# Optimization experiments

Measured on AMD Instinct MI355X. Metric: run time of the kernel, lower is better.

Reference implementation:

```python
import jax, jax.numpy as jnp
import numpy as np


def setup_inputs() -> dict:
    key = jax.random.key(0)
    ks = jax.random.split(key, 8)
    B, De, Do, T, H, W = 4, 128, 512, 4, 30, 52
    s = 0.05  # weight init scale
    return {
        "m_in": jax.random.normal(ks[0], (B, De, T, H, W), jnp.float32),
        "m_out": jax.random.normal(ks[1], (B, Do, T, H, W), jnp.float32),
        "q_in": jax.random.normal(ks[2], (B, De, H, W), jnp.float32),
        "q_out": jax.random.normal(ks[3], (B, Do, H, W), jnp.float32),
        "wr": jax.random.normal(ks[4], (Do, 2 * Do), jnp.float32) * s,
        "br": jnp.zeros((Do,), jnp.float32),
        "wu": jax.random.normal(ks[5], (Do, 2 * Do), jnp.float32) * s,
        "bu": jnp.zeros((Do,), jnp.float32),
        "wc": jax.random.normal(ks[6], (Do, 2 * Do), jnp.float32) * s,
        "bc": jnp.zeros((Do,), jnp.float32),
    }


def reference(m_in, m_out, q_in, q_out, wr, br, wu, bu, wc, bc):
    B, De, T, H, W = m_in.shape
    Do = m_out.shape[1]
    PROP_LAYERS = 5

    # --- memory read: pairwise frame attention (bmm + softmax + bmm) ---
    # keys: all T memory frames flattened; queries: current frame.
    mi = m_in.reshape(B, De, T * H * W)            # [B, De, THW]
    qi = q_in.reshape(B, De, H * W)                # [B, De, HW]
    p = jnp.einsum('bdk,bdq->bkq', mi, qi) / (De ** 0.5)  # [B, THW, HW]
    p = jax.nn.softmax(p, axis=1)                  # softmax over memory locations (dim=1 in torch)
    mem = jnp.einsum('bok,bkq->boq', m_out.reshape(B, Do, T * H * W), p)
    mem = mem.reshape(B, Do, H, W)                 # mem_mean; identical every propagate layer

    # --- ConvGRU_h (kernel_size=1 => per-pixel linear gates) ---
    def conv1x1(w, b, x):
        return jnp.einsum('oc,bchw->bohw', w, x) + b[None, :, None, None]

    def gru(x, h):
        xh = jnp.concatenate([x, h], axis=1)                       # [B, 2*Do, H, W]
        r = jax.nn.sigmoid(conv1x1(wr, br, xh))
        u = jax.nn.sigmoid(conv1x1(wu, bu, xh))
        c = jnp.tanh(conv1x1(wc, bc, jnp.concatenate([x, r * h], axis=1)))
        return h * (1.0 - u) + u * c

    q0 = q_out
    q = q_out
    for _ in range(PROP_LAYERS):
        q = gru(q, mem)  # original: q_out = ConvGRU_h(q_out, mem_mean)
    return jnp.concatenate([q, q0], axis=1)  # [B, 2*Do, H, W]
```

## Files before the change

### kernel.cpp

```cpp
#include <hip/hip_runtime.h>
#include <hip/hip_bf16.h>
#include <math.h>

typedef unsigned short u16;
typedef __attribute__((ext_vector_type(8))) short bf16x8;
typedef __attribute__((ext_vector_type(4))) float f32x4;

__device__ __forceinline__ u16 f2bf(float f) {
  union { float f; unsigned u; } x; x.f = f;
  unsigned r = x.u + 0x7fffu + ((x.u >> 16) & 1u);
  return (u16)(r >> 16);
}
__device__ __forceinline__ float bf2f(u16 h) {
  union { unsigned u; float f; } x; x.u = ((unsigned)h) << 16;
  return x.f;
}
__device__ __forceinline__ float sigmf(float x) {
  x = fminf(fmaxf(x, -30.f), 30.f);
  return 1.f / (1.f + __expf(-x));
}
__device__ __forceinline__ float tanh_fast(float x) {
  x = fminf(fmaxf(x, -15.f), 15.f);
  float t = __expf(2.f * x);
  return (t - 1.f) / (t + 1.f);
}

template<int N> __device__ __forceinline__ void wait_vmcnt() {
  if constexpr (N == 0)       asm volatile("s_waitcnt vmcnt(0)" ::: "memory");
  else if constexpr (N == 4)  asm volatile("s_waitcnt vmcnt(4)" ::: "memory");
  else if constexpr (N == 6)  asm volatile("s_waitcnt vmcnt(6)" ::: "memory");
  else if constexpr (N == 8)  asm volatile("s_waitcnt vmcnt(8)" ::: "memory");
  else static_assert(N == 0, "add vmcnt case");
}

#define NB 4
#define DE 128
#define DO_ 512
#define HW 1560
#define THW 6240
#define NP 1664
#define KP 6272
#define PROP 5
#define PVSPLIT 4
#define PVKC 1568
#define SCALE 0.08838834764831845f

template<int MODE, int BMT, int BKT>
__device__ __forceinline__
void gemm_core(const u16* __restrict__ A, const u16* __restrict__ Bt,
               int K, int lda, int ldb, long a_bs, long b_bs,
               void* __restrict__ out0v, long o0_bs, int ld0,
               u16* __restrict__ out1, long o1_bs, int ld1,
               u16* __restrict__ out2, long o2_bs,
               const void* __restrict__ e0v, long e0_bs,
               const void* __restrict__ e1v, long e1_bs,
               const void* __restrict__ e2v, long e2_bs,
               const void* __restrict__ e3v, long e3_bs,
               int nvalid, float scale)
{
  constexpr int WR = BMT / 64;
  constexpr int WC = 4 / WR;
  constexpr int NF = 8 / WC;
  constexpr int KK = BKT / 32;
  constexpr int ASLOT = BMT * BKT / 8;
  constexpr int BSLOT = 128 * BKT / 8;
  constexpr int NISS = (ASLOT + BSLOT) / 256;
  constexpr int RSH = (BMT == 128) ? 7 : 6;
  __shared__ u16 lds[2][ASLOT + BSLOT][8];

  const int tid = threadIdx.x;
  const int wave = tid >> 6, lane = tid & 63;
  const int kg = lane >> 4, lr = lane & 15;
  const int wrw = wave / WC, wcw = wave % WC;
  const long b = blockIdx.z;
  const int m0 = blockIdx.x * BMT, n0 = blockIdx.y * 128;
  A += b * a_bs; Bt += b * b_bs;

  float* out0f = (float*)out0v;
  u16* out0h = (u16*)out0v;
  const float* e0f = (const float*)e0v;
  const u16* e0h = (const u16*)e0v;
  const u16* e1h = (const u16*)e1v;
  const u16* e2h = (const u16*)e2v;
  const u16* e3h = (const u16*)e3v;

  auto stage = [&](int buf, int kt) {
#pragma unroll
    for (int i = 0; i < NISS; ++i) {
      int s = tid + 256 * i;
      const u16* src;
      if (s < ASLOT) {
        int row = s & (BMT - 1), g = s >> RSH;
        src = A + (long)(m0 + row) * lda + kt + g * 8;
      } else {
        int s2 = s - ASLOT;
        int row = s2 & 127, g = s2 >> 7;
        src = Bt + (long)(n0 + row) * ldb + kt + g * 8;
      }
      __builtin_amdgcn_global_load_lds(
          (const __attribute__((address_space(1))) void*)src,
          (__attribute__((address_space(3))) void*)&lds[buf][wave * 64 + 256 * i][0],
          16, 0, 0);
    }
  };

  f32x4 acc[4][NF];
#pragma unroll
  for (int m = 0; m < 4; ++m)
#pragma unroll
    for (int n = 0; n < NF; ++n) acc[m][n] = (f32x4){0.f, 0.f, 0.f, 0.f};

  const int nt = K / BKT;
  stage(0, 0);
  for (int t = 0; t < nt; ++t) {
    int cur = t & 1;
    if (t + 1 < nt) {
      stage(cur ^ 1, (t + 1) * BKT);
      wait_vmcnt<NISS>();
    } else {
      wait_vmcnt<0>();
    }
    __builtin_amdgcn_s_barrier();
    bf16x8 af[KK][4], bfr[KK][NF];
#pragma unroll
    for (int kk = 0; kk < KK; ++kk) {
#pragma unroll
      for (int m = 0; m < 4; ++m)
        af[kk][m] = *(const bf16x8*)&lds[cur][(kk * 4 + kg) * BMT + wrw * 64 + m * 16 + lr][0];
#pragma unroll
      for (int n = 0; n < NF; ++n)
        bfr[kk][n] = *(const bf16x8*)&lds[cur][ASLOT + (kk * 4 + kg) * 128 + (wcw * NF + n) * 16 + lr][0];
    }
#pragma unroll
    for (int kk = 0; kk < KK; ++kk)
#pragma unroll
      for (int m = 0; m < 4; ++m)
#pragma unroll
        for (int n = 0; n < NF; ++n)
          acc[m][n] = __builtin_amdgcn_mfma_f32_16x16x32_bf16(af[kk][m], bfr[kk][n], acc[m][n], 0, 0, 0);
    __builtin_amdgcn_s_barrier();
  }

#pragma unroll
  for (int m = 0; m < 4; ++m) {
    int rloc = wrw * 64 + m * 16 + kg * 4;
#pragma unroll
    for (int n = 0; n < NF; ++n) {
      int col = n0 + (wcw * NF + n) * 16 + lr;
#pragma unroll
      for (int j = 0; j < 4; ++j) {
        long row = m0 + rloc + j;
        float v = acc[m][n][j];
        if constexpr (MODE == 2) {
          out1[b * o1_bs + row * ld1 + col] = f2bf(v + e0f[col]);
        } else if constexpr (MODE == 3) {
          if (col < 1024) {
            float gt = sigmf(v + bf2f(e0h[b * e0_bs + row * 1024 + col]));
            if (col < 512)
              out1[b * o1_bs + row * ld1 + 512 + col] =
                  f2bf(gt * bf2f(e1h[b * e1_bs + row * 512 + col]));
            else
              out0h[b * o0_bs + row * ld0 + (col - 512)] = f2bf(gt);
          } else {
            out2[b * o2_bs + row * 512 + (col - 1024)] = f2bf(v);
          }
        } else if constexpr (MODE == 4) {
          float cg = tanh_fast(v + bf2f(e3h[b * e3_bs + row * 512 + col]) + e0f[col]);
          float u = bf2f(e1h[b * e1_bs + row * 512 + col]);
          float mm = bf2f(e2h[b * e2_bs + row * 512 + col]);
          float x = mm * (1.f - u) + u * cg;
          out1[b * o1_bs + row * ld1 + col] = f2bf(x);
          if (out0f && row < nvalid)
            out0f[b * o0_bs + (long)col * ld0 + row] = x;
        }
      }
    }
  }
}

#define GEMM_ARGS                                                              \
  const u16* __restrict__ A, const u16* __restrict__ Bt, int K, int lda,       \
  int ldb, long a_bs, long b_bs, void* __restrict__ out0v, long o0_bs,         \
  int ld0, u16* __restrict__ out1, long o1_bs, int ld1,                        \
  u16* __restrict__ out2, long o2_bs,                                          \
  const void* __restrict__ e0v, long e0_bs, const void* __restrict__ e1v,      \
  long e1_bs, const void* __restrict__ e2v, long e2_bs,                        \
  const void* __restrict__ e3v, long e3_bs, int nvalid, float scale
#define GEMM_PASS A, Bt, K, lda, ldb, a_bs, b_bs, out0v, o0_bs, ld0, out1,     \
  o1_bs, ld1, out2, o2_bs, e0v, e0_bs, e1v, e1_bs, e2v, e2_bs, e3v, e3_bs,     \
  nvalid, scale

__global__ __launch_bounds__(256) void gk_chru(GEMM_ARGS)   { gemm_core<2, 64, 64>(GEMM_PASS); }
__global__ __launch_bounds__(256) void gk_gates(GEMM_ARGS)  { gemm_core<3, 128, 64>(GEMM_PASS); }
__global__ __launch_bounds__(256) void gk_cand(GEMM_ARGS)   { gemm_core<4, 64, 64>(GEMM_PASS); }

__global__ __launch_bounds__(256, 2)
void gemm_fa(const u16* __restrict__ qiT, const u16* __restrict__ miT,
             const u16* __restrict__ moutb,
             u16* __restrict__ Ppart, float* __restrict__ Zp)
{
  const int bid = blockIdx.x;
  const int xcd = bid & 7, i = bid >> 3;
  const int s = xcd * 52 + i;
  const int pair = s / 26, mb = s - pair * 26;
  const int b = pair >> 2, z = pair & 3;
  const int m0 = mb * 64;
  const int k0 = z * PVKC;

  const int tid = threadIdx.x;
  const int wave = tid >> 6, lane = tid & 63;
  const int kg = lane >> 4, lr = lane & 15;

  __shared__ u16 ldsQ[1024 * 8];
  __shared__ u16 ldsK[2][512 * 8];
  __shared__ u16 ldsP[64 * 40];

  const u16* Qb = qiT + (long)b * NP * DE;
  const u16* Mb = miT + (long)b * KP * DE;
  const u16* B0 = moutb + (long)b * DO_ * KP +
                  (long)(wave * 128 + lr) * KP + kg * 8;

  auto stageK = [&](int buf, int ts) {
#pragma unroll
    for (int i2 = 0; i2 < 2; ++i2) {
      int s2 = tid + 256 * i2;
      int row = s2 & 31, g = s2 >> 5;
      const u16* src = Mb + (long)(k0 + ts * 32 + row) * DE + g * 8;
      __builtin_amdgcn_global_load_lds(
          (const __attribute__((address_space(1))) void*)src,
          (__attribute__((address_space(3))) void*)&ldsK[buf][(wave * 64 + 256 * i2) * 8],
          16, 0, 0);
    }
  };

#pragma unroll
  for (int i2 = 0; i2 < 4; ++i2) {
    int s2 = tid + 256 * i2;
    int row = s2 & 63, g = s2 >> 6;
    const u16* src = Qb + (long)(m0 + row) * DE + g * 8;
    __builtin_amdgcn_global_load_lds(
        (const __attribute__((address_space(1))) void*)src,
        (__attribute__((address_space(3))) void*)&ldsQ[(wave * 64 + 256 * i2) * 8],
        16, 0, 0);
  }
  stageK(0, 0);
  __syncthreads();

  f32x4 acc[4][8];
#pragma unroll
  for (int m = 0; m < 4; ++m)
#pragma unroll
    for (int n = 0; n < 8; ++n) acc[m][n] = (f32x4){0.f, 0.f, 0.f, 0.f};
  float zacc[4] = {0.f, 0.f, 0.f, 0.f};
  bf16x8 b_[8];

#define FA_STEP(T, CUR, DOS)                                                     \
  {                                                                              \
    _Pragma("unroll") for (int n = 0; n < 8; ++n)                                \
        b_[n] = *(const bf16x8*)&B0[(long)n * 16 * KP + k0 + (T) * 32];          \
    if (DOS) stageK((CUR) ^ 1, (T) + 1);                                         \
    bf16x8 qf[4], kc[2][4];                                                      \
    _Pragma("unroll") for (int kk = 0; kk < 4; ++kk)                             \
        qf[kk] = *(const bf16x8*)&ldsQ[((kk * 4 + kg) * 64 + wave * 16 + lr) * 8]; \
    _Pragma("unroll") for (int n = 0; n < 2; ++n)                                \
        _Pragma("unroll") for (int kk = 0; kk < 4; ++kk)                         \
            kc[n][kk] = *(const bf16x8*)&ldsK[CUR][((kk * 4 + kg) * 32 + n * 16 + lr) * 8]; \
    f32x4 sacc[2];                                                               \
    sacc[0] = (f32x4){0.f, 0.f, 0.f, 0.f};                                       \
    sacc[1] = (f32x4){0.f, 0.f, 0.f, 0.f};                                       \
    _Pragma("unroll") for (int kk = 0; kk < 4; ++kk)                             \
        _Pragma("unroll") for (int n = 0; n < 2; ++n)                            \
            sacc[n] = __builtin_amdgcn_mfma_f32_16x16x32_bf16(qf[kk], kc[n][kk], \
                                                              sacc[n], 0, 0, 0); \
    _Pragma("unroll") for (int n = 0; n < 2; ++n) {                              \
      bool valid = (k0 + (T) * 32 + n * 16 + lr) < THW;                          \
      _Pragma("unroll") for (int j = 0; j < 4; ++j) {                            \
        float pf = valid ? __expf(sacc[n][j] * SCALE) : 0.f;                     \
        zacc[j] += pf;                                                           \
        ldsP[(wave * 16 + kg * 4 + j) * 40 + n * 16 + lr] = f2bf(pf);            \
      }                                                                          \
    }                                                                            \
    if (DOS) asm volatile("s_waitcnt vmcnt(2) lgkmcnt(0)" ::: "memory");         \
    else     asm volatile("s_waitcnt vmcnt(0) lgkmcnt(0)" ::: "memory");         \
    __builtin_amdgcn_s_barrier();                                                \
    bf16x8 pa[4];                                                                \
    _Pragma("unroll") for (int m = 0; m < 4; ++m)                                \
        pa[m] = *(const bf16x8*)&ldsP[(m * 16 + lr) * 40 + kg * 8];              \
    _Pragma("unroll") for (int m = 0; m < 4; ++m)                                \
        _Pragma("unroll") for (int n = 0; n < 8; ++n)                            \
            acc[m][n] = __builtin_amdgcn_mfma_f32_16x16x32_bf16(pa[m], b_[n],    \
                                                                acc[m][n], 0, 0, 0); \
    asm volatile("s_waitcnt vmcnt(0) lgkmcnt(0)" ::: "memory");                  \
    __builtin_amdgcn_s_barrier();                                                \
  }

  for (int tp = 0; tp < 24; ++tp) {
    FA_STEP(2 * tp, 0, 1);
    FA_STEP(2 * tp + 1, 1, 1);
  }
  FA_STEP(48, 0, 0);
#undef FA_STEP

#pragma unroll
  for (int j = 0; j < 4; ++j) {
#pragma unroll
    for (int msk = 1; msk < 16; msk <<= 1)
      zacc[j] += __shfl_xor(zacc[j], msk, 64);
  }
  if (lr == 0) {
#pragma unroll
    for (int j = 0; j < 4; ++j)
      Zp[((long)b * PVSPLIT + z) * NP + m0 + wave * 16 + kg * 4 + j] = zacc[j];
  }

  u16* out = Ppart + (long)(b * PVSPLIT + z) * NP * DO_;
#pragma unroll
  for (int m = 0; m < 4; ++m) {
#pragma unroll
    for (int n = 0; n < 8; ++n) {
      int col = wave * 128 + n * 16 + lr;
#pragma unroll
      for (int j = 0; j < 4; ++j) {
        int row = m0 + m * 16 + kg * 4 + j;
        out[(long)row * DO_ + col] = f2bf(acc[m][n][j]);
      }
    }
  }
}

__global__ void k_transpose_cast(const float* __restrict__ in, u16* __restrict__ out,
                                 int R, int C, int Cp, int out_ld,
                                 long in_bs, long out_bs) {
  __shared__ float t[32][33];
  long b = blockIdx.z;
  int c0 = blockIdx.x * 32, r0 = blockIdx.y * 32;
  int tx = threadIdx.x, ty = threadIdx.y;
#pragma unroll
  for (int i = 0; i < 32; i += 8) {
    int r = r0 + ty + i, c = c0 + tx;
    t[ty + i][tx] = (r < R && c < C) ? in[b * in_bs + (long)r * C + c] : 0.f;
  }
  __syncthreads();
#pragma unroll
  for (int i = 0; i < 32; i += 8) {
    int c = c0 + ty + i, r = r0 + tx;
    if (c < Cp && r < R)
      out[b * out_bs + (long)c * out_ld + r] = f2bf(t[tx][ty + i]);
  }
}

__global__ void k_cast_pad4(const float* __restrict__ in, u16* __restrict__ out,
                            int Cin, int Cout, long in_bs, long out_bs) {
  int c4 = (blockIdx.x * 256 + threadIdx.x) * 4;
  int r = blockIdx.y;
  long b = blockIdx.z;
  if (c4 >= Cout) return;
  uint2 o = {0u, 0u};
  if (c4 < Cin) {
    float4 v = *(const float4*)&in[b * in_bs + (long)r * Cin + c4];
    o.x = (unsigned)f2bf(v.x) | ((unsigned)f2bf(v.y) << 16);
    o.y = (unsigned)f2bf(v.z) | ((unsigned)f2bf(v.w) << 16);
  }
  *(uint2*)&out[b * out_bs + (long)r * Cout + c4] = o;
}

__global__ void k_build_w(const float* __restrict__ wr_, const float* __restrict__ wu_,
                          const float* __restrict__ wc_,
                          u16* __restrict__ wruh, u16* __restrict__ wruxc,
                          u16* __restrict__ wch) {
  int k = blockIdx.x * 256 + threadIdx.x;
  int m = blockIdx.y;
  if (k >= 512) return;
  if (m < 1024) {
    const float* src = (m < 512) ? wr_ : wu_;
    wruh[m * 512 + k] = f2bf(src[(m & 511) * 1024 + 512 + k]);
  } else if (m < 2560) {
    int n = m - 1024;
    const float* src = (n < 512) ? wr_ : ((n < 1024) ? wu_ : wc_);
    wruxc[n * 512 + k] = f2bf(src[(n & 511) * 1024 + k]);
  } else {
    int n = m - 2560;
    wch[n * 512 + k] = f2bf(wc_[n * 1024 + 512 + k]);
  }
}

__global__ void k_bias_ru(const float* __restrict__ br_, const float* __restrict__ bu_,
                          float* __restrict__ bias) {
  int i = blockIdx.x * 256 + threadIdx.x;
  if (i < 1024) bias[i] = (i < 512) ? br_[i] : bu_[i - 512];
}

__global__ void k_reduce_mem(const u16* __restrict__ Ppart, const float* __restrict__ Zp,
                             u16* __restrict__ memTb) {
  long t = (long)blockIdx.x * 256 + threadIdx.x;
  const long bs = (long)NP * DO_;
  if (t >= (long)NB * bs / 8) return;
  long flat = t * 8;
  int b = (int)(flat / bs);
  long r = flat - (long)b * bs;
  int q = (int)(r / DO_);
  float s[8];
#pragma unroll
  for (int e = 0; e < 8; ++e) s[e] = 0.f;
  float zs = 0.f;
#pragma unroll
  for (int z = 0; z < PVSPLIT; ++z) {
    uint4 v = *(const uint4*)&Ppart[(long)(b * PVSPLIT + z) * bs + r];
    s[0] += bf2f((u16)(v.x & 0xffff)); s[1] += bf2f((u16)(v.x >> 16));
    s[2] += bf2f((u16)(v.y & 0xffff)); s[3] += bf2f((u16)(v.y >> 16));
    s[4] += bf2f((u16)(v.z & 0xffff)); s[5] += bf2f((u16)(v.z >> 16));
    s[6] += bf2f((u16)(v.w & 0xffff)); s[7] += bf2f((u16)(v.w >> 16));
    zs += Zp[((long)b * PVSPLIT + z) * NP + q];
  }
  float iz = 1.f / zs;
  uint4 o;
  o.x = (unsigned)f2bf(s[0] * iz) | ((unsigned)f2bf(s[1] * iz) << 16);
  o.y = (unsigned)f2bf(s[2] * iz) | ((unsigned)f2bf(s[3] * iz) << 16);
  o.z = (unsigned)f2bf(s[4] * iz) | ((unsigned)f2bf(s[5] * iz) << 16);
  o.w = (unsigned)f2bf(s[6] * iz) | ((unsigned)f2bf(s[7] * iz) << 16);
  *(uint4*)&memTb[(long)b * bs + r] = o;
}

__global__ void k_copy_q0(const float4* __restrict__ src, float4* __restrict__ dst) {
  int idx = blockIdx.x * 256 + threadIdx.x;
  long b = blockIdx.z;
  const long n4 = (long)DO_ * HW / 4;
  if (idx < n4)
    dst[b * ((long)1024 * HW / 4) + n4 + idx] = src[b * n4 + idx];
}

extern "C" void kernel_launch(void* const* d_in, const int* in_sizes, int n_in,
                              void* d_out, int out_size, void* d_ws, size_t ws_size,
                              hipStream_t stream) {
  const float* m_in  = (const float*)d_in[0];
  const float* m_out = (const float*)d_in[1];
  const float* q_in  = (const float*)d_in[2];
  const float* q_out = (const float*)d_in[3];
  const float* wr    = (const float*)d_in[4];
  const float* br    = (const float*)d_in[5];
  const float* wu    = (const float*)d_in[6];
  const float* bu    = (const float*)d_in[7];
  const float* wc    = (const float*)d_in[8];
  const float* bc    = (const float*)d_in[9];
  float* dout = (float*)d_out;

  char* p = (char*)d_ws;
  size_t off = 0;
  auto alloc = [&](size_t bytes) { void* r = p + off; off += (bytes + 255) & ~(size_t)255; return r; };
  u16*   miT    = (u16*)alloc((size_t)NB * KP * DE * 2);
  u16*   qiT    = (u16*)alloc((size_t)NB * NP * DE * 2);
  float* Zp     = (float*)alloc((size_t)NB * PVSPLIT * NP * 4);
  u16*   moutb  = (u16*)alloc((size_t)NB * DO_ * KP * 2);
  u16*   memTb  = (u16*)alloc((size_t)NB * NP * DO_ * 2);
  u16*   chru   = (u16*)alloc((size_t)NB * NP * 1024 * 2);
  u16*   U      = (u16*)alloc((size_t)NB * NP * DO_ * 2);
  u16*   XRb    = (u16*)alloc((size_t)NB * NP * 1024 * 2);
  float* Qfin   = (float*)alloc((size_t)NB * NP * DO_ * 4);
  (void)Qfin;
  u16*   XRa    = (u16*)alloc((size_t)NB * NP * 1024 * 2);
  u16*   Cx     = (u16*)alloc((size_t)NB * NP * 512 * 2);
  u16*   wruh   = (u16*)alloc((size_t)1024 * 512 * 2);
  u16*   wruxc  = (u16*)alloc((size_t)1536 * 512 * 2);
  u16*   wch    = (u16*)alloc((size_t)512 * 512 * 2);
  float* biasru = (float*)alloc((size_t)1024 * 4);
  u16*   Ppart  = (u16*)chru;
  if (off > ws_size) return;

  k_build_w<<<dim3(2, 3072), 256, 0, stream>>>(wr, wu, wc, wruh, wruxc, wch);
  k_bias_ru<<<dim3(4), 256, 0, stream>>>(br, bu, biasru);
  k_cast_pad4<<<dim3(7, 512, NB), 256, 0, stream>>>(
      m_out, moutb, THW, KP, (long)DO_ * THW, (long)DO_ * KP);
  k_transpose_cast<<<dim3(196, 4, NB), dim3(32, 8), 0, stream>>>(
      m_in, miT, DE, THW, KP, DE, (long)DE * THW, (long)KP * DE);
  k_transpose_cast<<<dim3(52, 4, NB), dim3(32, 8), 0, stream>>>(
      q_in, qiT, DE, HW, NP, DE, (long)DE * HW, (long)NP * DE);
  k_transpose_cast<<<dim3(52, 16, NB), dim3(32, 8), 0, stream>>>(
      q_out, XRa, DO_, HW, NP, 1024, (long)DO_ * HW, (long)NP * 1024);

  gemm_fa<<<dim3(416), 256, 0, stream>>>(qiT, miT, moutb, Ppart, Zp);
  k_reduce_mem<<<dim3(1664), 256, 0, stream>>>(Ppart, Zp, memTb);

  gk_chru<<<dim3(26, 8, NB), 256, 0, stream>>>(
      memTb, wruh, DO_, DO_, DO_, (long)NP * DO_, 0,
      nullptr, 0, 0, chru, (long)NP * 1024, 1024, nullptr, 0,
      biasru, 0, nullptr, 0, nullptr, 0, nullptr, 0, 0, 0.f);

  u16* xr[2] = {XRa, XRb};
  for (int l = 0; l < PROP; ++l) {
    u16* cur = xr[l & 1];
    u16* nxt = xr[(l + 1) & 1];
    gk_gates<<<dim3(13, 12, NB), 256, 0, stream>>>(
        cur, wruxc, DO_, 1024, DO_, (long)NP * 1024, 0,
        U, (long)NP * DO_, DO_, cur, (long)NP * 1024, 1024,
        Cx, (long)NP * 512,
        chru, (long)NP * 1024, memTb, (long)NP * DO_, nullptr, 0,
        nullptr, 0, 0, 0.f);
    gk_cand<<<dim3(26, 4, NB), 256, 0, stream>>>(
        cur + 512, wch, DO_, 1024, DO_, (long)NP * 1024, 0,
        (l == PROP - 1) ? (void*)dout : nullptr, (long)1024 * HW, HW,
        nxt, (long)NP * 1024, 1024, nullptr, 0,
        bc, 0, U, (long)NP * DO_, memTb, (long)NP * DO_,
        Cx, (long)NP * 512, HW, 0.f);
  }

  k_copy_q0<<<dim3(780, 1, NB), 256, 0, stream>>>((const float4*)q_out, (float4*)dout);
}
```

Baseline: 627.8 us.

## Triple-buffer K tiles in attention kernel and fold bias setup into weight build

The fused attention GEMM kernel now keeps three LDS buffers for key tiles and prefetches two steps ahead. This lets it drop the trailing full vmcnt(0) wait and barrier pair in each step, and replaces the initial __syncthreads with a partial vmcnt wait. Separately, the bias-concatenation kernel is merged into the weight-build kernel, saving one launch. The extra LDS buffer raises shared memory per block and may reduce occupancy, and the hand-set waitcnt values must match the actual number of in-flight loads.

Measured after the change: 632.7 us. About the same (+0.8%).

```diff
diff --git a/kernel.cpp b/kernel.cpp
--- a/kernel.cpp
+++ b/kernel.cpp
@@ -212,7 +212,7 @@
   const int kg = lane >> 4, lr = lane & 15;
 
   __shared__ u16 ldsQ[1024 * 8];
-  __shared__ u16 ldsK[2][512 * 8];
+  __shared__ u16 ldsK[3][512 * 8];
   __shared__ u16 ldsP[64 * 40];
 
   const u16* Qb = qiT + (long)b * NP * DE;
@@ -244,7 +244,7 @@
         16, 0, 0);
   }
   stageK(0, 0);
-  __syncthreads();
+  stageK(1, 1);
 
   f32x4 acc[4][8];
 #pragma unroll
@@ -254,11 +254,15 @@
   float zacc[4] = {0.f, 0.f, 0.f, 0.f};
   bf16x8 b_[8];
 
-#define FA_STEP(T, CUR, DOS)                                                     \
+#define FA_STEP(T, CUR, SBUF, DOS, FIRST, VMMID)                                 \
   {                                                                              \
     _Pragma("unroll") for (int n = 0; n < 8; ++n)                                \
         b_[n] = *(const bf16x8*)&B0[(long)n * 16 * KP + k0 + (T) * 32];          \
-    if (DOS) stageK((CUR) ^ 1, (T) + 1);                                         \
+    if (DOS) stageK(SBUF, (T) + 2);                                              \
+    if (FIRST) {                                                                 \
+      asm volatile("s_waitcnt vmcnt(12)" ::: "memory");                          \
+      __builtin_amdgcn_s_barrier();                                              \
+    }                                                                            \
     bf16x8 qf[4], kc[2][4];                                                      \
     _Pragma("unroll") for (int kk = 0; kk < 4; ++kk)                             \
         qf[kk] = *(const bf16x8*)&ldsQ[((kk * 4 + kg) * 64 + wave * 16 + lr) * 8]; \
@@ -280,8 +284,8 @@
         ldsP[(wave * 16 + kg * 4 + j) * 40 + n * 16 + lr] = f2bf(pf);            \
       }                                                                          \
     }                                                                            \
-    if (DOS) asm volatile("s_waitcnt vmcnt(2) lgkmcnt(0)" ::: "memory");         \
-    else     asm volatile("s_waitcnt vmcnt(0) lgkmcnt(0)" ::: "memory");         \
+    if (VMMID == 2) asm volatile("s_waitcnt vmcnt(2) lgkmcnt(0)" ::: "memory");  \
+    else            asm volatile("s_waitcnt vmcnt(0) lgkmcnt(0)" ::: "memory");  \
     __builtin_amdgcn_s_barrier();                                                \
     bf16x8 pa[4];                                                                \
     _Pragma("unroll") for (int m = 0; m < 4; ++m)                                \
@@ -290,15 +294,18 @@
         _Pragma("unroll") for (int n = 0; n < 8; ++n)                            \
             acc[m][n] = __builtin_amdgcn_mfma_f32_16x16x32_bf16(pa[m], b_[n],    \
                                                                 acc[m][n], 0, 0, 0); \
-    asm volatile("s_waitcnt vmcnt(0) lgkmcnt(0)" ::: "memory");                  \
     __builtin_amdgcn_s_barrier();                                                \
   }
 
-  for (int tp = 0; tp < 24; ++tp) {
-    FA_STEP(2 * tp, 0, 1);
-    FA_STEP(2 * tp + 1, 1, 1);
-  }
-  FA_STEP(48, 0, 0);
+  FA_STEP(0, 0, 2, 1, 1, 2);
+  FA_STEP(1, 1, 0, 1, 0, 2);
+  FA_STEP(2, 2, 1, 1, 0, 2);
+  for (int t3 = 1; t3 < 16; ++t3) {
+    FA_STEP(3 * t3 + 0, 0, 2, 1, 0, 2);
+    FA_STEP(3 * t3 + 1, 1, 0, 1, 0, 2);
+    FA_STEP(3 * t3 + 2, 2, 1, 1, 0, 2);
+  }
+  FA_STEP(48, 0, 0, 0, 0, 0);
 #undef FA_STEP
 
 #pragma unroll
@@ -366,11 +373,13 @@
 
 __global__ void k_build_w(const float* __restrict__ wr_, const float* __restrict__ wu_,
                           const float* __restrict__ wc_,
+                          const float* __restrict__ br_, const float* __restrict__ bu_,
                           u16* __restrict__ wruh, u16* __restrict__ wruxc,
-                          u16* __restrict__ wch) {
+                          u16* __restrict__ wch, float* __restrict__ bias) {
   int k = blockIdx.x * 256 + threadIdx.x;
   int m = blockIdx.y;
   if (k >= 512) return;
+  if (m < 2) bias[m * 512 + k] = (m == 0) ? br_[k] : bu_[k];
   if (m < 1024) {
     const float* src = (m < 512) ? wr_ : wu_;
     wruh[m * 512 + k] = f2bf(src[(m & 511) * 1024 + 512 + k]);
@@ -382,12 +391,6 @@
     int n = m - 2560;
     wch[n * 512 + k] = f2bf(wc_[n * 1024 + 512 + k]);
   }
-}
-
-__global__ void k_bias_ru(const float* __restrict__ br_, const float* __restrict__ bu_,
-                          float* __restrict__ bias) {
-  int i = blockIdx.x * 256 + threadIdx.x;
-  if (i < 1024) bias[i] = (i < 512) ? br_[i] : bu_[i - 512];
 }
 
 __global__ void k_reduce_mem(const u16* __restrict__ Ppart, const float* __restrict__ Zp,
@@ -466,8 +469,8 @@
   u16*   Ppart  = (u16*)chru;
   if (off > ws_size) return;
 
-  k_build_w<<<dim3(2, 3072), 256, 0, stream>>>(wr, wu, wc, wruh, wruxc, wch);
-  k_bias_ru<<<dim3(4), 256, 0, stream>>>(br, bu, biasru);
+  k_build_w<<<dim3(2, 3072), 256, 0, stream>>>(wr, wu, wc, br, bu,
+                                               wruh, wruxc, wch, biasru);
   k_cast_pad4<<<dim3(7, 512, NB), 256, 0, stream>>>(
       m_out, moutb, THW, KP, (long)DO_ * THW, (long)DO_ * KP);
   k_transpose_cast<<<dim3(196, 4, NB), dim3(32, 8), 0, stream>>>(
```
